# Kernel tuning notes

Hardware: AMD Instinct MI355X
Metric: run time of the kernel (lower is better)

Reference implementation:

```python
import jax, jax.numpy as jnp
import numpy as np

B, C, T, V = 32, 96, 256, 25
BC = C // 4   # TCN branch channels
E = C // 4    # adyn embed dim (max(C//4, 8))


def hswish(x):
    return x * jnp.clip(x + 3.0, 0.0, 6.0) / 6.0


def bn(x, p):
    # p: [4, c] = (gamma, beta, running_mean, running_var); x: [B, c, T, V]
    g, b, rm, rv = p[0], p[1], p[2], p[3]
    inv = jax.lax.rsqrt(rv + 1e-5)
    return (x - rm[:, None, None]) * (g * inv)[:, None, None] + b[:, None, None]


def conv1x1(x, w):
    # w: [O, I]
    return jnp.einsum('bctv,oc->botv', x, w)


def tconv(x, w, stride, dil):
    # temporal conv, kernel 3 on T axis; w: [O, I, 3]
    return jax.lax.conv_general_dilated(
        x, w[:, :, :, None], window_strides=(stride, 1),
        padding=((dil, dil), (0, 0)), rhs_dilation=(dil, 1),
        dimension_numbers=('NCHW', 'OIHW', 'NCHW'))


def _forward(x, A_gcn, W_gcn, gcn_bn, Wp, W_adyn, adyn_gate,
             se_w1, se_b1, se_w2, se_b2,
             pa_w, pa_bn, ta_w, ta_bn, pb_w, pb_bn, tb_w, tb_bn,
             pc_w, pc_bn, pd_w, pd_bn, intra_idx, inter_idx):
    res = x
    # --- BRASP: channel-cyclic shift along joint axis (Shift-GCN style) ---
    sh = (jnp.arange(V)[None, :] + jnp.arange(C)[:, None]) % V  # [C, V]
    x = jnp.take_along_axis(x, sh[None, :, None, :], axis=3)
    # --- SGPShift: half channels gather via intra neighbors, half via inter ---
    h = C // 2
    x = jnp.concatenate([x[:, :h][..., intra_idx], x[:, h:][..., inter_idx]], axis=1)
    # --- multi-partition graph conv: y = mean_k Conv1x1_k(x @ A_k) ---
    xa = jnp.einsum('bctv,kvw->kbctw', x, A_gcn)           # [K,B,C,T,V]
    y = jnp.einsum('kbctw,koc->botw', xa, W_gcn) / A_gcn.shape[0]
    # --- dynamic adjacency (adyn) ---
    emb = jnp.einsum('bcv,ec->bev', x.mean(axis=2), Wp)    # proj then mean over T (linear)
    emb = emb / (jnp.linalg.norm(emb, axis=1, keepdims=True) + 1e-12)
    A_dyn = jnp.einsum('bev,bew->bvw', emb, emb)           # [B,V,V]
    x_dyn = jnp.einsum('bctv,bvw->bctw', x, A_dyn)
    y = y + jax.nn.sigmoid(adyn_gate) * conv1x1(x_dyn, W_adyn)
    x = hswish(bn(y, gcn_bn))
    # --- ChannelSE ---
    s = x.mean(axis=(2, 3))                                 # [B, C]
    z = jax.nn.sigmoid(jnp.dot(jax.nn.relu(jnp.dot(s, se_w1.T) + se_b1), se_w2.T) + se_b2)
    x = x * z[:, :, None, None]
    # --- MultiScaleTCN (stride 1, 4 branches of C//4 channels) ---
    a = hswish(bn(conv1x1(x, pa_w), pa_bn))
    a = bn(tconv(a, ta_w, 1, 1), ta_bn)
    b_ = hswish(bn(conv1x1(x, pb_w), pb_bn))
    b_ = bn(tconv(b_, tb_w, 1, 2), tb_bn)
    c_ = bn(conv1x1(x, pc_w), pc_bn)
    c_ = jax.lax.reduce_window(c_, -jnp.inf, jax.lax.max,
                               (1, 1, 3, 1), (1, 1, 1, 1),
                               [(0, 0), (0, 0), (1, 1), (0, 0)])
    d_ = bn(conv1x1(x, pd_w), pd_bn)
    xt = jnp.concatenate([a, b_, c_, d_], axis=1)           # [B, C, T, V]
    # --- residual + out activation (in==out, stride 1 -> identity residual) ---
    return hswish(xt + res)


def setup_inputs() -> dict:
    key = jax.random.key(0)
    ks = jax.random.split(key, 24)

    def n(k, shape, s=0.1):
        return jax.random.normal(k, shape, jnp.float32) * s

    def mkbn(k, c):
        k1, k2, k3, k4 = jax.random.split(k, 4)
        return jnp.stack([1.0 + 0.1 * jax.random.normal(k1, (c,)),
                          0.1 * jax.random.normal(k2, (c,)),
                          0.1 * jax.random.normal(k3, (c,)),
                          0.5 + jax.random.uniform(k4, (c,))])

    A = jax.random.uniform(ks[1], (3, V, V))
    A = A / (A.sum(-1, keepdims=True) + 1e-6)  # row-normalized structural adjacencies
    return dict(
        x=jax.random.normal(ks[0], (B, C, T, V), jnp.float32),
        intra_idx=jax.random.randint(ks[2], (V,), 0, V),
        inter_idx=jax.random.randint(ks[3], (V,), 0, V),
        A_gcn=A,
        W_gcn=n(ks[4], (3, C, C)),
        gcn_bn=mkbn(ks[5], C),
        Wp=n(ks[6], (E, C)),
        W_adyn=n(ks[7], (C, C)),
        adyn_gate=jnp.float32(-4.0),
        se_w1=n(ks[8], (BC, C)), se_b1=jnp.zeros((BC,), jnp.float32),
        se_w2=n(ks[9], (C, BC)), se_b2=jnp.zeros((C,), jnp.float32),
        pa_w=n(ks[10], (BC, C)), pa_bn=mkbn(ks[11], BC),
        ta_w=n(ks[12], (BC, BC, 3)), ta_bn=mkbn(ks[13], BC),
        pb_w=n(ks[14], (BC, C)), pb_bn=mkbn(ks[15], BC),
        tb_w=n(ks[16], (BC, BC, 3)), tb_bn=mkbn(ks[17], BC),
        pc_w=n(ks[18], (BC, C)), pc_bn=mkbn(ks[19], BC),
        pd_w=n(ks[20], (BC, C)), pd_bn=mkbn(ks[21], BC),
    )


def reference(x, intra_idx, inter_idx, A_gcn, W_gcn, gcn_bn, Wp, W_adyn, adyn_gate,
              se_w1, se_b1, se_w2, se_b2,
              pa_w, pa_bn, ta_w, ta_bn, pb_w, pb_bn, tb_w, tb_bn,
              pc_w, pc_bn, pd_w, pd_bn):
    return _forward(x, A_gcn, W_gcn, gcn_bn, Wp, W_adyn, adyn_gate,
                    se_w1, se_b1, se_w2, se_b2,
                    pa_w, pa_bn, ta_w, ta_bn, pb_w, pb_bn, tb_w, tb_bn,
                    pc_w, pc_bn, pd_w, pd_bn, intra_idx, inter_idx)
```

## Files before the change

### kernel.cpp

```cpp
#include <hip/hip_runtime.h>
#include <math.h>

#define NB 32
#define NC 96
#define NT 256
#define NV 25
#define NBC 24
#define NE 24
#define CV (NC * NV)
#define EV (NE * NV)
#define NK4 384
#define NN 6400
#define ACOLS 112
#define APAD 40
#define XAP 104

typedef __attribute__((ext_vector_type(8))) short bf16x8;
typedef __attribute__((ext_vector_type(4))) float f32x4;

__device__ __forceinline__ float hswish(float x) {
    return x * fminf(fmaxf(x + 3.f, 0.f), 6.f) * (1.f / 6.f);
}
__device__ __forceinline__ float bnval(float x, const float* p, int n, int c) {
    return (x - p[2 * n + c]) * p[c] * rsqrtf(p[3 * n + c] + 1e-5f) + p[n + c];
}
__device__ __forceinline__ unsigned short f2bf(float f) {
    unsigned u = __float_as_uint(f);
    u += 0x7fffu + ((u >> 16) & 1u);
    return (unsigned short)(u >> 16);
}
__device__ __forceinline__ float bf2f(unsigned short us) {
    return __uint_as_float((unsigned)us << 16);
}

__global__ __launch_bounds__(256) void k_mean(const float* __restrict__ x,
                                              const int* __restrict__ intra,
                                              const int* __restrict__ inter,
                                              float* __restrict__ xm,
                                              unsigned short* __restrict__ xsh) {
    int bc = blockIdx.x;
    int c = bc % NC;
    int tid = threadIdx.x;
    __shared__ int colL[NV];
    if (tid < NV) {
        int s0 = (c < NC / 2) ? intra[tid] : inter[tid];
        colL[tid] = (s0 + c) % NV;
    }
    __syncthreads();
    const float* xp = x + (size_t)bc * NT * NV + (size_t)tid * NV;
    float a[NV];
#pragma unroll
    for (int v = 0; v < NV; ++v) a[v] = xp[v];
    unsigned short row[32];
#pragma unroll
    for (int v = 0; v < NV; ++v) row[v] = f2bf(a[colL[v]]);
#pragma unroll
    for (int v = NV; v < 32; ++v) row[v] = 0;
    bf16x8* dst = (bf16x8*)(xsh + ((size_t)bc * NT + tid) * 32);
#pragma unroll
    for (int s = 0; s < 4; ++s) dst[s] = ((bf16x8*)row)[s];
    __shared__ float part[4][NV];
    int lane = tid & 63, wid = tid >> 6;
#pragma unroll
    for (int v = 0; v < NV; ++v) {
        float val = a[v];
        for (int off = 32; off > 0; off >>= 1) val += __shfl_down(val, off, 64);
        if (lane == 0) part[wid][v] = val;
    }
    __syncthreads();
    if (tid < NV) {
        float s = part[0][tid] + part[1][tid] + part[2][tid] + part[3][tid];
        xm[bc * NV + tid] = s * (1.0f / NT);
    }
}

__global__ __launch_bounds__(256) void k_adyn(const float* __restrict__ xm,
                                              const float* __restrict__ Wp,
                                              const int* __restrict__ intra,
                                              const int* __restrict__ inter,
                                              const float* __restrict__ Agcn,
                                              const float* __restrict__ gate,
                                              unsigned short* __restrict__ acat) {
    int b = blockIdx.x, tid = threadIdx.x;
    __shared__ float xms[CV];
    __shared__ float embs[EV];
    __shared__ float nrm[NV];
    __shared__ float Ads[NV * NV];
    for (int i = tid; i < CV; i += 256) xms[i] = xm[b * CV + i];
    __syncthreads();
    for (int i = tid; i < EV; i += 256) {
        int e = i / NV, v = i % NV;
        int iv = intra[v], ev2 = inter[v];
        float acc = 0.f;
        for (int c = 0; c < NC; ++c) {
            int s0 = (c < NC / 2) ? iv : ev2;
            int col = (s0 + c) % NV;
            acc = fmaf(xms[c * NV + col], Wp[e * NC + c], acc);
        }
        embs[e * NV + v] = acc;
    }
    __syncthreads();
    if (tid < NV) {
        float acc = 0.f;
        for (int e = 0; e < NE; ++e) {
            float t = embs[e * NV + tid];
            acc = fmaf(t, t, acc);
        }
        nrm[tid] = sqrtf(acc) + 1e-12f;
    }
    __syncthreads();
    for (int i = tid; i < NV * NV; i += 256) {
        int v = i / NV, w = i % NV;
        float acc = 0.f;
        for (int e = 0; e < NE; ++e)
            acc = fmaf(embs[e * NV + v], embs[e * NV + w], acc);
        Ads[i] = acc / (nrm[v] * nrm[w]);
    }
    __syncthreads();
    float sg = 1.f / (1.f + expf(-gate[0]));
    for (int i = tid; i < ACOLS * APAD; i += 256) {
        int col = i / APAD, v = i % APAD;
        float val = 0.f;
        if (col < 100 && v < NV) {
            int j = col / NV, w = col % NV;
            if (j < 3) val = Agcn[(j * NV + v) * NV + w] * (1.f / 3.f);
            else val = sg * Ads[v * NV + w];
        }
        acat[(size_t)b * ACOLS * APAD + i] = f2bf(val);
    }
}

__global__ __launch_bounds__(256) void k_wcat(const float* __restrict__ Wg,
                                              const float* __restrict__ Wa,
                                              unsigned short* __restrict__ wcat) {
    int i = blockIdx.x * 256 + threadIdx.x;
    if (i >= NC * NK4) return;
    int o = i / NK4, kc = i % NK4;
    int j = kc / NC, c = kc % NC;
    float v = (j < 3) ? Wg[(j * NC + o) * NC + c] : Wa[o * NC + c];
    wcat[i] = f2bf(v);
}

__global__ __launch_bounds__(256) void k_twp(const float* __restrict__ ta_w,
                                             const float* __restrict__ tb_w,
                                             unsigned short* __restrict__ wtw) {
    int i = blockIdx.x * 256 + threadIdx.x;
    if (i >= 2 * 32 * 96) return;
    int br = i / (32 * 96), rem = i % (32 * 96);
    int o = rem / 96, k = rem % 96;
    float v = 0.f;
    if (o < 24 && k < 72) {
        int i3 = k / 24, c2 = k % 24;
        v = (br ? tb_w : ta_w)[(o * 24 + c2) * 3 + i3];
    }
    wtw[i] = f2bf(v);
}

__global__ __launch_bounds__(256) void k_gcn2(const unsigned short* __restrict__ xsh,
                                              const unsigned short* __restrict__ acat,
                                              const unsigned short* __restrict__ wcat,
                                              const float* __restrict__ gbn,
                                              unsigned short* __restrict__ x3) {
    int blk = blockIdx.x;
    int b = blk >> 6, tg = blk & 63;
    int t0 = tg * 4;
    int tid = threadIdx.x;
    __shared__ __align__(16) unsigned short Xa[112 * XAP];
    int lane = tid & 63, wv = tid >> 6;
    int lr = lane & 15, kg = lane >> 4;
    f32x4 acc[6][2];
#pragma unroll
    for (int mt = 0; mt < 6; ++mt)
#pragma unroll
        for (int q = 0; q < 2; ++q) acc[mt][q] = (f32x4){0.f, 0.f, 0.f, 0.f};

    const unsigned short* acb = acat + (size_t)b * ACOLS * APAD;
    const unsigned short* xsb = xsh + (size_t)b * NC * NT * 32;

    for (int j = 0; j < 4; ++j) {
        __syncthreads();
        bf16x8 af0 = *(const bf16x8*)(acb + (j * NV + lr) * APAD + kg * 8);
        bf16x8 af1 = *(const bf16x8*)(acb + (j * NV + 16 + lr) * APAD + kg * 8);
        int cB = lr >> 2, tl = lr & 3;
#pragma unroll
        for (int q = 0; q < 6; ++q) {
            int c = (wv * 6 + q) * 4 + cB;
            bf16x8 bf = *(const bf16x8*)(xsb + ((size_t)c * NT + t0 + tl) * 32 + kg * 8);
            f32x4 z = {0.f, 0.f, 0.f, 0.f};
            f32x4 c0 = __builtin_amdgcn_mfma_f32_16x16x32_bf16(af0, bf, z, 0, 0, 0);
            f32x4 c1 = __builtin_amdgcn_mfma_f32_16x16x32_bf16(af1, bf, z, 0, 0, 0);
            int base = tl * NV;
#pragma unroll
            for (int i = 0; i < 4; ++i) {
                int w = kg * 4 + i;
                Xa[(base + w) * XAP + c] = f2bf(c0[i]);
            }
#pragma unroll
            for (int i = 0; i < 4; ++i) {
                int w = 16 + kg * 4 + i;
                if (w < NV) Xa[(base + w) * XAP + c] = f2bf(c1[i]);
            }
        }
        __syncthreads();
        const unsigned short* wj = wcat + j * NC + lr * NK4 + kg * 8;
#pragma unroll
        for (int kt = 0; kt < 3; ++kt) {
            bf16x8 af[6];
#pragma unroll
            for (int mt = 0; mt < 6; ++mt)
                af[mt] = *(const bf16x8*)(wj + mt * 16 * NK4 + kt * 32);
#pragma unroll
            for (int q = 0; q < 2; ++q) {
                int nf = wv * 2 + q;
                if (nf < 7) {
                    bf16x8 bf = *(const bf16x8*)&Xa[(nf * 16 + lr) * XAP + (kt * 4 + kg) * 8];
#pragma unroll
                    for (int mt = 0; mt < 6; ++mt)
                        acc[mt][q] = __builtin_amdgcn_mfma_f32_16x16x32_bf16(af[mt], bf, acc[mt][q], 0, 0, 0);
                }
            }
        }
    }
#pragma unroll
    for (int q = 0; q < 2; ++q) {
        int nf = wv * 2 + q;
        int nl = nf * 16 + lr;
        if (nf < 7 && nl < 100) {
            size_t nbase = (size_t)b * NC * NN + tg * 100 + nl;
#pragma unroll
            for (int mt = 0; mt < 6; ++mt) {
#pragma unroll
                for (int i = 0; i < 4; ++i) {
                    int o = mt * 16 + kg * 4 + i;
                    float val = hswish(bnval(acc[mt][q][i], gbn, NC, o));
                    x3[nbase + (size_t)o * NN] = f2bf(val);
                }
            }
        }
    }
}

__global__ __launch_bounds__(256) void k_sred(const unsigned short* __restrict__ x3,
                                              float* __restrict__ s) {
    int bc = blockIdx.x, tid = threadIdx.x;
    const unsigned short* p = x3 + (size_t)bc * NT * NV;
    float acc = 0.f;
    for (int i = tid; i < NN / 8; i += 256) {
        bf16x8 v = *(const bf16x8*)(p + i * 8);
#pragma unroll
        for (int e = 0; e < 8; ++e) acc += bf2f((unsigned short)v[e]);
    }
    for (int off = 32; off > 0; off >>= 1) acc += __shfl_down(acc, off, 64);
    __shared__ float part[4];
    if ((tid & 63) == 0) part[tid >> 6] = acc;
    __syncthreads();
    if (tid == 0) s[bc] = (part[0] + part[1] + part[2] + part[3]) / (float)(NT * NV);
}

__global__ __launch_bounds__(128) void k_se(const float* __restrict__ s,
                                            const float* __restrict__ w1,
                                            const float* __restrict__ b1,
                                            const float* __restrict__ w2,
                                            const float* __restrict__ b2,
                                            float* __restrict__ z) {
    int b = blockIdx.x, tid = threadIdx.x;
    __shared__ float sl[NC], hl[NBC];
    if (tid < NC) sl[tid] = s[b * NC + tid];
    __syncthreads();
    if (tid < NBC) {
        float acc = b1[tid];
        for (int c = 0; c < NC; ++c) acc = fmaf(w1[tid * NC + c], sl[c], acc);
        hl[tid] = fmaxf(acc, 0.f);
    }
    __syncthreads();
    if (tid < NC) {
        float acc = b2[tid];
        for (int j = 0; j < NBC; ++j) acc = fmaf(w2[tid * NBC + j], hl[j], acc);
        z[b * NC + tid] = 1.f / (1.f + expf(-acc));
    }
}

__global__ __launch_bounds__(256) void k_pww(const float* __restrict__ z,
                                             const float* __restrict__ pa_w,
                                             const float* __restrict__ pb_w,
                                             const float* __restrict__ pc_w,
                                             const float* __restrict__ pd_w,
                                             unsigned short* __restrict__ wse) {
    int i = blockIdx.x * 256 + threadIdx.x;
    if (i >= NB * NC * NC) return;
    int b = i / (NC * NC), rem = i % (NC * NC);
    int o = rem / NC, c = rem % NC;
    int br = o / NBC, lc = o % NBC;
    const float* P = (br == 0) ? pa_w : (br == 1) ? pb_w : (br == 2) ? pc_w : pd_w;
    wse[i] = f2bf(P[lc * NC + c] * z[b * NC + c]);
}

__global__ __launch_bounds__(256) void k_pwg(const unsigned short* __restrict__ x3,
                                             const unsigned short* __restrict__ wse,
                                             const float* __restrict__ pa_bn,
                                             const float* __restrict__ pb_bn,
                                             const float* __restrict__ pc_bn,
                                             const float* __restrict__ pd_bn,
                                             unsigned short* __restrict__ ut48,
                                             unsigned short* __restrict__ u2) {
    int blk = blockIdx.x;
    int b = blk / 50;
    int n0 = (blk % 50) * 128;
    int tid = threadIdx.x;
    __shared__ __align__(16) char SMEM[33280];
    unsigned short* Wpan = (unsigned short*)SMEM;
    unsigned short* Xp = Wpan + 3 * NC * APAD;
    float* Yt = (float*)SMEM;

    int lane = tid & 63, wv = tid >> 6;
    int lr = lane & 15, kg = lane >> 4;
    f32x4 acc[6][2];
#pragma unroll
    for (int mt = 0; mt < 6; ++mt)
#pragma unroll
        for (int nn = 0; nn < 2; ++nn) acc[mt][nn] = (f32x4){0.f, 0.f, 0.f, 0.f};

    const unsigned short* wb = wse + (size_t)b * NC * NC;
    for (int i = tid; i < 3 * NC * 4; i += 256) {
        int kt = i / (NC * 4), rem = i % (NC * 4);
        int o = rem >> 2, s4 = rem & 3;
        *(bf16x8*)&Wpan[(kt * NC + o) * APAD + s4 * 8] =
            *(const bf16x8*)(wb + o * NC + kt * 32 + s4 * 8);
    }

    int kp = tid >> 4;
    int seg = tid & 15;
    const unsigned short* x3b = x3 + (size_t)b * NC * NN;

    for (int kt = 0; kt < 3; ++kt) {
        int k0 = kt * 32;
        {
            const unsigned short* src0 = x3b + (size_t)(k0 + 2 * kp) * NN + n0 + seg * 8;
            bf16x8 va = *(const bf16x8*)src0;
            bf16x8 vb = *(const bf16x8*)(src0 + NN);
            char* base = (char*)Xp;
#pragma unroll
            for (int e = 0; e < 8; ++e) {
                int n = seg * 8 + e;
                int g = (kp >> 2) ^ (n & 3) ^ ((n >> 3) & 3);
                unsigned pk = (unsigned)(unsigned short)va[e] |
                              ((unsigned)(unsigned short)vb[e] << 16);
                *(unsigned*)(base + n * 80 + g * 16 + (kp & 3) * 4) = pk;
            }
        }
        __syncthreads();
        bf16x8 afr[6];
#pragma unroll
        for (int mt = 0; mt < 6; ++mt)
            afr[mt] = *(const bf16x8*)&Wpan[(kt * NC + mt * 16 + lr) * APAD + kg * 8];
#pragma unroll
        for (int nn = 0; nn < 2; ++nn) {
            int nl = (wv * 2 + nn) * 16 + lr;
            int g = kg ^ (nl & 3) ^ ((nl >> 3) & 3);
            bf16x8 bb = *(const bf16x8*)((const char*)Xp + nl * 80 + g * 16);
#pragma unroll
            for (int mt = 0; mt < 6; ++mt)
                acc[mt][nn] = __builtin_amdgcn_mfma_f32_16x16x32_bf16(afr[mt], bb, acc[mt][nn], 0, 0, 0);
        }
        __syncthreads();
    }
#pragma unroll
    for (int mt = 0; mt < 6; ++mt)
#pragma unroll
        for (int nn = 0; nn < 2; ++nn) {
            int nl = (wv * 2 + nn) * 16 + lr;
#pragma unroll
            for (int i = 0; i < 4; ++i) {
                int o = mt * 16 + kg * 4 + i;
                int br = o / NBC, lc = o % NBC;
                const float* bnp = (br == 0) ? pa_bn : (br == 1) ? pb_bn
                                 : (br == 2) ? pc_bn : pd_bn;
                float val = bnval(acc[mt][nn][i], bnp, NBC, lc);
                if (br < 2) {
                    Yt[nl * 49 + o] = hswish(val);
                } else {
                    u2[((size_t)b * 48 + (o - 48)) * NN + n0 + nl] = f2bf(val);
                }
            }
        }
    __syncthreads();
    for (int i = tid; i < 128 * 6; i += 256) {
        int n = i / 6, og = i % 6;
        bf16x8 v;
#pragma unroll
        for (int e = 0; e < 8; ++e) v[e] = (short)f2bf(Yt[n * 49 + og * 8 + e]);
        *(bf16x8*)(ut48 + ((size_t)b * NN + n0 + n) * 48 + og * 8) = v;
    }
}

__global__ __launch_bounds__(256) void k_tcnm(const unsigned short* __restrict__ ut48,
                                              const unsigned short* __restrict__ wtw,
                                              const float* __restrict__ ta_bn,
                                              const float* __restrict__ tb_bn,
                                              unsigned short* __restrict__ uc) {
    int blk = blockIdx.x;
    int b = blk / 50, n0 = (blk % 50) * 128;
    int tid = threadIdx.x;
    __shared__ __align__(16) unsigned short Ut[240][56];
    int wn = n0 - 56;
    const unsigned short* utb = ut48 + (size_t)b * NN * 48;
    for (int idx = tid; idx < 240 * 6; idx += 256) {
        int row = idx / 6, seg = idx % 6;
        int n = wn + row;
        bf16x8 val = {0, 0, 0, 0, 0, 0, 0, 0};
        if (n >= 0 && n < NN)
            val = *(const bf16x8*)(utb + (size_t)n * 48 + seg * 8);
        *(bf16x8*)&Ut[row][seg * 8] = val;
    }
    int lane = tid & 63, wave = tid >> 6;
    int lr = lane & 15, kg = lane >> 4;
    int br = wave >> 1, mh = wave & 1;
    int dn = 25 + br * 25;
    bf16x8 af[3];
#pragma unroll
    for (int kt = 0; kt < 3; ++kt)
        af[kt] = *(const bf16x8*)(wtw + (br * 32 + mh * 16 + lr) * 96 + kt * 32 + kg * 8);
    __syncthreads();

    f32x4 acc[8];
#pragma unroll
    for (int nt = 0; nt < 8; ++nt) acc[nt] = (f32x4){0.f, 0.f, 0.f, 0.f};
#pragma unroll
    for (int kt = 0; kt < 3; ++kt) {
        int g = kt * 4 + kg;
        int gg = (g > 8) ? 8 : g;
        int i3 = gg / 3;
        int c2b = (gg - i3 * 3) * 8;
        int roff = 56 + (i3 - 1) * dn;
        int colb = br * 24 + c2b;
#pragma unroll
        for (int nt = 0; nt < 8; ++nt) {
            int nrow = nt * 16 + lr + roff;
            bf16x8 bb = *(const bf16x8*)&Ut[nrow][colb];
            acc[nt] = __builtin_amdgcn_mfma_f32_16x16x32_bf16(af[kt], bb, acc[nt], 0, 0, 0);
        }
    }
    const float* bnp = br ? tb_bn : ta_bn;
    int ml = mh * 16 + kg * 4;
#pragma unroll
    for (int ii = 0; ii < 4; ++ii) {
        int ol = ml + ii;
        if (ol < 24) {
            int oc = br * 24 + ol;
#pragma unroll
            for (int nt = 0; nt < 8; ++nt) {
                int n = n0 + nt * 16 + lr;
                uc[((size_t)b * 48 + oc) * NN + n] = f2bf(bnval(acc[nt][ii], bnp, NBC, ol));
            }
        }
    }
}

__global__ __launch_bounds__(256) void k_fin(const unsigned short* __restrict__ uc,
                                             const unsigned short* __restrict__ u2,
                                             const float* __restrict__ x,
                                             float* __restrict__ out) {
    const int JV = NN / 8;
    const int NVEC = NB * NC * JV;
    for (int vid = blockIdx.x * 256 + threadIdx.x; vid < NVEC; vid += gridDim.x * 256) {
        int j = vid % JV;
        int bc = vid / JV;
        int ch = bc % NC, b = bc / NC;
        int n = j * 8;
        float val[8];
        if (ch < 48) {
            bf16x8 t = *(const bf16x8*)(uc + ((size_t)b * 48 + ch) * NN + n);
#pragma unroll
            for (int e = 0; e < 8; ++e) val[e] = bf2f((unsigned short)t[e]);
        } else if (ch < 72) {
            const unsigned short* p = u2 + ((size_t)b * 48 + (ch - 48)) * NN;
            if (j >= 4 && j <= JV - 5) {
                bf16x8 M = *(const bf16x8*)(p + n);
                bf16x8 Lm = *(const bf16x8*)(p + n - 24);
                bf16x8 Rp = *(const bf16x8*)(p + n + 24);
                float lm1 = bf2f(p[n - 25]);
                float rp1 = bf2f(p[n + 32]);
#pragma unroll
                for (int e = 0; e < 8; ++e) {
                    float vm = (e == 0) ? lm1 : bf2f((unsigned short)Lm[e - 1]);
                    float vp = (e == 7) ? rp1 : bf2f((unsigned short)Rp[e + 1]);
                    val[e] = fmaxf(fmaxf(bf2f((unsigned short)M[e]), vm), vp);
                }
            } else {
#pragma unroll
                for (int e = 0; e < 8; ++e) {
                    int ne = n + e;
                    float m = bf2f(p[ne]);
                    if (ne >= 25) m = fmaxf(m, bf2f(p[ne - 25]));
                    if (ne + 25 < NN) m = fmaxf(m, bf2f(p[ne + 25]));
                    val[e] = m;
                }
            }
        } else {
            bf16x8 t = *(const bf16x8*)(u2 + ((size_t)b * 48 + (ch - 48)) * NN + n);
#pragma unroll
            for (int e = 0; e < 8; ++e) val[e] = bf2f((unsigned short)t[e]);
        }
        const float* xp = x + (size_t)bc * NN + n;
        float* op = out + (size_t)bc * NN + n;
        f32x4 x0 = *(const f32x4*)xp;
        f32x4 x1 = *(const f32x4*)(xp + 4);
        f32x4 o0, o1;
#pragma unroll
        for (int e = 0; e < 4; ++e) o0[e] = hswish(val[e] + x0[e]);
#pragma unroll
        for (int e = 0; e < 4; ++e) o1[e] = hswish(val[e + 4] + x1[e]);
        *(f32x4*)op = o0;
        *(f32x4*)(op + 4) = o1;
    }
}

extern "C" void kernel_launch(void* const* d_in, const int* in_sizes, int n_in,
                              void* d_out, int out_size, void* d_ws, size_t ws_size,
                              hipStream_t stream) {
    const float* x = (const float*)d_in[0];
    const int* intra = (const int*)d_in[1];
    const int* inter = (const int*)d_in[2];
    const float* A_gcn = (const float*)d_in[3];
    const float* W_gcn = (const float*)d_in[4];
    const float* gcn_bn = (const float*)d_in[5];
    const float* Wp = (const float*)d_in[6];
    const float* W_adyn = (const float*)d_in[7];
    const float* gate = (const float*)d_in[8];
    const float* se_w1 = (const float*)d_in[9];
    const float* se_b1 = (const float*)d_in[10];
    const float* se_w2 = (const float*)d_in[11];
    const float* se_b2 = (const float*)d_in[12];
    const float* pa_w = (const float*)d_in[13];
    const float* pa_bn = (const float*)d_in[14];
    const float* ta_w = (const float*)d_in[15];
    const float* ta_bn = (const float*)d_in[16];
    const float* pb_w = (const float*)d_in[17];
    const float* pb_bn = (const float*)d_in[18];
    const float* tb_w = (const float*)d_in[19];
    const float* tb_bn = (const float*)d_in[20];
    const float* pc_w = (const float*)d_in[21];
    const float* pc_bn = (const float*)d_in[22];
    const float* pd_w = (const float*)d_in[23];
    const float* pd_bn = (const float*)d_in[24];
    float* out = (float*)d_out;

    char* wsb = (char*)d_ws;
    const size_t ELEMS = (size_t)NB * NC * NT * NV;
    const size_t HALF = (size_t)NB * NN * 48;
    const size_t XSH = (size_t)NB * NC * NT * 32;
    unsigned short* x3 = (unsigned short*)wsb;
    unsigned short* ut48 = x3 + ELEMS;
    unsigned short* u2 = ut48 + HALF;
    unsigned short* uc = u2 + HALF;
    unsigned short* xsh = uc + HALF;
    float* xm = (float*)(xsh + XSH);
    float* sb = xm + NB * NC * NV;
    float* zb = sb + NB * NC;
    unsigned short* wcat = (unsigned short*)(zb + NB * NC);
    unsigned short* acat = wcat + NC * NK4;
    unsigned short* wse = acat + NB * ACOLS * APAD;
    unsigned short* wtw = wse + (size_t)NB * NC * NC;

    k_mean<<<NB * NC, 256, 0, stream>>>(x, intra, inter, xm, xsh);
    k_adyn<<<NB, 256, 0, stream>>>(xm, Wp, intra, inter, A_gcn, gate, acat);
    k_wcat<<<(NC * NK4 + 255) / 256, 256, 0, stream>>>(W_gcn, W_adyn, wcat);
    k_twp<<<(2 * 32 * 96 + 255) / 256, 256, 0, stream>>>(ta_w, tb_w, wtw);
    k_gcn2<<<NB * 64, 256, 0, stream>>>(xsh, acat, wcat, gcn_bn, x3);
    k_sred<<<NB * NC, 256, 0, stream>>>(x3, sb);
    k_se<<<NB, 128, 0, stream>>>(sb, se_w1, se_b1, se_w2, se_b2, zb);
    k_pww<<<(NB * NC * NC + 255) / 256, 256, 0, stream>>>(zb, pa_w, pb_w, pc_w, pd_w, wse);
    k_pwg<<<NB * 50, 256, 0, stream>>>(x3, wse, pa_bn, pb_bn, pc_bn, pd_bn, ut48, u2);
    k_tcnm<<<NB * 50, 256, 0, stream>>>(ut48, wtw, ta_bn, tb_bn, uc);
    k_fin<<<2048, 256, 0, stream>>>(uc, u2, x, out);
}
```

Before: 255.8 us.

## Double-buffer LDS in gcn2 and process eight time steps per block

```diff
diff --git a/kernel.cpp b/kernel.cpp
--- a/kernel.cpp
+++ b/kernel.cpp
@@ -13,7 +13,8 @@
 #define NN 6400
 #define ACOLS 112
 #define APAD 40
-#define XAP 104
+#define XAP 100
+#define XAHALF (100 * XAP)
 
 typedef __attribute__((ext_vector_type(8))) short bf16x8;
 typedef __attribute__((ext_vector_type(4))) float f32x4;
@@ -162,82 +163,100 @@
                                               const float* __restrict__ gbn,
                                               unsigned short* __restrict__ x3) {
     int blk = blockIdx.x;
-    int b = blk >> 6, tg = blk & 63;
-    int t0 = tg * 4;
+    int b = blk >> 5, tg = blk & 31;
+    int t0 = tg * 8;
     int tid = threadIdx.x;
-    __shared__ __align__(16) unsigned short Xa[112 * XAP];
+    __shared__ __align__(16) unsigned short Xa[2 * XAHALF];
     int lane = tid & 63, wv = tid >> 6;
     int lr = lane & 15, kg = lane >> 4;
-    f32x4 acc[6][2];
+    f32x4 acc[6][2][2];
 #pragma unroll
     for (int mt = 0; mt < 6; ++mt)
 #pragma unroll
-        for (int q = 0; q < 2; ++q) acc[mt][q] = (f32x4){0.f, 0.f, 0.f, 0.f};
+        for (int h = 0; h < 2; ++h)
+#pragma unroll
+            for (int q = 0; q < 2; ++q) acc[mt][h][q] = (f32x4){0.f, 0.f, 0.f, 0.f};
 
     const unsigned short* acb = acat + (size_t)b * ACOLS * APAD;
     const unsigned short* xsb = xsh + (size_t)b * NC * NT * 32;
-
-    for (int j = 0; j < 4; ++j) {
+    int cB = lr >> 2, tl = lr & 3;
+
+    for (int p = 0; p <= 8; ++p) {
         __syncthreads();
-        bf16x8 af0 = *(const bf16x8*)(acb + (j * NV + lr) * APAD + kg * 8);
-        bf16x8 af1 = *(const bf16x8*)(acb + (j * NV + 16 + lr) * APAD + kg * 8);
-        int cB = lr >> 2, tl = lr & 3;
-#pragma unroll
-        for (int q = 0; q < 6; ++q) {
-            int c = (wv * 6 + q) * 4 + cB;
-            bf16x8 bf = *(const bf16x8*)(xsb + ((size_t)c * NT + t0 + tl) * 32 + kg * 8);
-            f32x4 z = {0.f, 0.f, 0.f, 0.f};
-            f32x4 c0 = __builtin_amdgcn_mfma_f32_16x16x32_bf16(af0, bf, z, 0, 0, 0);
-            f32x4 c1 = __builtin_amdgcn_mfma_f32_16x16x32_bf16(af1, bf, z, 0, 0, 0);
-            int base = tl * NV;
-#pragma unroll
-            for (int i = 0; i < 4; ++i) {
-                int w = kg * 4 + i;
-                Xa[(base + w) * XAP + c] = f2bf(c0[i]);
-            }
-#pragma unroll
-            for (int i = 0; i < 4; ++i) {
-                int w = 16 + kg * 4 + i;
-                if (w < NV) Xa[(base + w) * XAP + c] = f2bf(c1[i]);
-            }
-        }
-        __syncthreads();
-        const unsigned short* wj = wcat + j * NC + lr * NK4 + kg * 8;
-#pragma unroll
-        for (int kt = 0; kt < 3; ++kt) {
-            bf16x8 af[6];
-#pragma unroll
-            for (int mt = 0; mt < 6; ++mt)
-                af[mt] = *(const bf16x8*)(wj + mt * 16 * NK4 + kt * 32);
-#pragma unroll
-            for (int q = 0; q < 2; ++q) {
-                int nf = wv * 2 + q;
-                if (nf < 7) {
-                    bf16x8 bf = *(const bf16x8*)&Xa[(nf * 16 + lr) * XAP + (kt * 4 + kg) * 8];
-#pragma unroll
-                    for (int mt = 0; mt < 6; ++mt)
-                        acc[mt][q] = __builtin_amdgcn_mfma_f32_16x16x32_bf16(af[mt], bf, acc[mt][q], 0, 0, 0);
-                }
-            }
-        }
-    }
-#pragma unroll
-    for (int q = 0; q < 2; ++q) {
-        int nf = wv * 2 + q;
-        int nl = nf * 16 + lr;
-        if (nf < 7 && nl < 100) {
-            size_t nbase = (size_t)b * NC * NN + tg * 100 + nl;
-#pragma unroll
-            for (int mt = 0; mt < 6; ++mt) {
+        if (p < 8) {
+            int j = p >> 1, h = p & 1;
+            unsigned short* XaW = Xa + (p & 1) * XAHALF;
+            bf16x8 af0 = *(const bf16x8*)(acb + (j * NV + lr) * APAD + kg * 8);
+            bf16x8 af1 = *(const bf16x8*)(acb + (j * NV + 16 + lr) * APAD + kg * 8);
+#pragma unroll
+            for (int q = 0; q < 6; ++q) {
+                int c = (wv * 6 + q) * 4 + cB;
+                bf16x8 bf = *(const bf16x8*)(xsb + ((size_t)c * NT + t0 + h * 4 + tl) * 32 + kg * 8);
+                f32x4 z = {0.f, 0.f, 0.f, 0.f};
+                f32x4 c0 = __builtin_amdgcn_mfma_f32_16x16x32_bf16(af0, bf, z, 0, 0, 0);
+                f32x4 c1 = __builtin_amdgcn_mfma_f32_16x16x32_bf16(af1, bf, z, 0, 0, 0);
+                int base = tl * NV;
 #pragma unroll
                 for (int i = 0; i < 4; ++i) {
-                    int o = mt * 16 + kg * 4 + i;
-                    float val = hswish(bnval(acc[mt][q][i], gbn, NC, o));
-                    x3[nbase + (size_t)o * NN] = f2bf(val);
-                }
-            }
-        }
-    }
+                    int w = kg * 4 + i;
+                    XaW[(base + w) * XAP + c] = f2bf(c0[i]);
+                }
+#pragma unroll
+                for (int i = 0; i < 4; ++i) {
+                    int w = 16 + kg * 4 + i;
+                    if (w < NV) XaW[(base + w) * XAP + c] = f2bf(c1[i]);
+                }
+            }
+        }
+        if (p >= 1) {
+            int jh = p - 1;
+            int j = jh >> 1, h = jh & 1;
+            const unsigned short* XaR = Xa + (jh & 1) * XAHALF;
+            const unsigned short* wj = wcat + j * NC + lr * NK4 + kg * 8;
+#pragma unroll
+            for (int kt = 0; kt < 3; ++kt) {
+                bf16x8 af[6];
+#pragma unroll
+                for (int mt = 0; mt < 6; ++mt)
+                    af[mt] = *(const bf16x8*)(wj + mt * 16 * NK4 + kt * 32);
+#pragma unroll
+                for (int q = 0; q < 2; ++q) {
+                    int nf = wv * 2 + q;
+                    if (nf < 7) {
+                        int rowq = nf * 16 + lr;
+                        bf16x8 bf;
+                        if (rowq < 100) {
+                            bf = *(const bf16x8*)&XaR[rowq * XAP + (kt * 4 + kg) * 8];
+                        } else {
+                            bf = (bf16x8){0, 0, 0, 0, 0, 0, 0, 0};
+                        }
+#pragma unroll
+                        for (int mt = 0; mt < 6; ++mt)
+                            acc[mt][h][q] = __builtin_amdgcn_mfma_f32_16x16x32_bf16(af[mt], bf, acc[mt][h][q], 0, 0, 0);
+                    }
+                }
+            }
+        }
+    }
+#pragma unroll
+    for (int h = 0; h < 2; ++h)
+#pragma unroll
+        for (int q = 0; q < 2; ++q) {
+            int nf = wv * 2 + q;
+            int nl = nf * 16 + lr;
+            if (nf < 7 && nl < 100) {
+                size_t nbase = (size_t)b * NC * NN + tg * 200 + h * 100 + nl;
+#pragma unroll
+                for (int mt = 0; mt < 6; ++mt) {
+#pragma unroll
+                    for (int i = 0; i < 4; ++i) {
+                        int o = mt * 16 + kg * 4 + i;
+                        float val = hswish(bnval(acc[mt][h][q][i], gbn, NC, o));
+                        x3[nbase + (size_t)o * NN] = f2bf(val);
+                    }
+                }
+            }
+        }
 }
 
 __global__ __launch_bounds__(256) void k_sred(const unsigned short* __restrict__ x3,
@@ -566,7 +585,7 @@
     k_adyn<<<NB, 256, 0, stream>>>(xm, Wp, intra, inter, A_gcn, gate, acat);
     k_wcat<<<(NC * NK4 + 255) / 256, 256, 0, stream>>>(W_gcn, W_adyn, wcat);
     k_twp<<<(2 * 32 * 96 + 255) / 256, 256, 0, stream>>>(ta_w, tb_w, wtw);
-    k_gcn2<<<NB * 64, 256, 0, stream>>>(xsh, acat, wcat, gcn_bn, x3);
+    k_gcn2<<<NB * 32, 256, 0, stream>>>(xsh, acat, wcat, gcn_bn, x3);
     k_sred<<<NB * NC, 256, 0, stream>>>(x3, sb);
     k_se<<<NB, 128, 0, stream>>>(sb, se_w1, se_b1, se_w2, se_b2, zb);
     k_pww<<<(NB * NC * NC + 255) / 256, 256, 0, stream>>>(zb, pa_w, pb_w, pc_w, pd_w, wse);
```

Measured after the change: 493.7 us. 93.0% more time.
